# Optimization experiments

Hardware: AMD Instinct MI355X
Metric: run time of the kernel (lower is better)

The kernel has to match this reference:

```python
import jax, jax.numpy as jnp
import numpy as np

D, H, K, L, F, G, M, OUT = 1280, 16, 80, 4, 5120, 48, 2, 2048
HALF = K // 2  # rotary half dim = 40


def _token_coords(grid_thw, merge_size, N):
    tpi = grid_thw[:, 0] * grid_thw[:, 1] * grid_thw[:, 2]
    cu = jnp.concatenate([jnp.zeros(1, jnp.int32), jnp.cumsum(tpi).astype(jnp.int32)])
    tok = jnp.arange(N, dtype=jnp.int32)
    img_id = jnp.searchsorted(cu[1:], tok, side='right')
    local = tok - cu[img_id]
    h = grid_thw[img_id, 1]
    w = grid_thw[img_id, 2]
    spatial = local % (h * w)
    msq = merge_size * merge_size
    mw = w // merge_size
    group, intra = spatial // msq, spatial % msq
    row = (group // mw) * merge_size + intra // merge_size
    col = (group % mw) * merge_size + intra % merge_size
    return row, col, h, w, cu


def _layernorm(x, s, b, eps=1e-6):
    mu = jnp.mean(x, -1, keepdims=True)
    var = jnp.mean(jnp.square(x - mu), -1, keepdims=True)
    return (x - mu) * jax.lax.rsqrt(var + eps) * s + b


def _rotate_half(x):
    x1, x2 = x[..., :HALF], x[..., HALF:]
    return jnp.concatenate([-x2, x1], axis=-1)


def setup_inputs() -> dict:
    key = jax.random.key(0)
    ks = jax.random.split(key, 16)
    s = 0.02
    inp = {
        'pixels': jax.random.normal(ks[0], (2048, 1536), jnp.float32),
        'grid_thw': jnp.array([[1, 16, 32]] * 4, jnp.int32),
        'pos_embed': jax.random.normal(ks[1], (G * G, D), jnp.float32) * s,
        'patch_w': jax.random.normal(ks[2], (1536, D), jnp.float32) * s,
        'patch_b': jnp.zeros((D,), jnp.float32),
        'ln1_s': jnp.ones((L, D), jnp.float32), 'ln1_b': jnp.zeros((L, D), jnp.float32),
        'qkv_w': jax.random.normal(ks[3], (L, D, 3 * D), jnp.float32) * s,
        'qkv_b': jnp.zeros((L, 3 * D), jnp.float32),
        'proj_w': jax.random.normal(ks[4], (L, D, D), jnp.float32) * s,
        'proj_b': jnp.zeros((L, D), jnp.float32),
        'ln2_s': jnp.ones((L, D), jnp.float32), 'ln2_b': jnp.zeros((L, D), jnp.float32),
        'fc1_w': jax.random.normal(ks[5], (L, D, F), jnp.float32) * s,
        'fc1_b': jnp.zeros((L, F), jnp.float32),
        'fc2_w': jax.random.normal(ks[6], (L, F, D), jnp.float32) * s,
        'fc2_b': jnp.zeros((L, D), jnp.float32),
        'm_norm_s': jnp.ones((D,), jnp.float32), 'm_norm_b': jnp.zeros((D,), jnp.float32),
        'm_fc1_w': jax.random.normal(ks[7], (D * M * M, D * M * M), jnp.float32) * s,
        'm_fc1_b': jnp.zeros((D * M * M,), jnp.float32),
        'm_fc2_w': jax.random.normal(ks[8], (D * M * M, OUT), jnp.float32) * s,
        'm_fc2_b': jnp.zeros((OUT,), jnp.float32),
    }
    return inp


def _forward(pixels, grid_thw, pos_embed, patch_w, patch_b, ln1_s, ln1_b, qkv_w, qkv_b,
             proj_w, proj_b, ln2_s, ln2_b, fc1_w, fc1_b, fc2_w, fc2_b,
             m_norm_s, m_norm_b, m_fc1_w, m_fc1_b, m_fc2_w, m_fc2_b):
    N = pixels.shape[0]
    row, col, h, w, cu = _token_coords(grid_thw, M, N)

    # patch embed: conv with stride==kernel over flattened patches == linear
    x = pixels @ patch_w + patch_b  # [N, D]

    # bilinear position-embedding interpolation onto each image's (h, w) grid
    rf = jnp.where(h > 1, row.astype(jnp.float32) * (G - 1) / jnp.maximum(h - 1, 1), 0.0)
    cf = jnp.where(w > 1, col.astype(jnp.float32) * (G - 1) / jnp.maximum(w - 1, 1), 0.0)
    r0 = jnp.floor(rf).astype(jnp.int32); r1 = jnp.minimum(r0 + 1, G - 1)
    c0 = jnp.floor(cf).astype(jnp.int32); c1 = jnp.minimum(c0 + 1, G - 1)
    wr = (rf - r0)[:, None]; wc = (cf - c0)[:, None]
    pe = (pos_embed[r0 * G + c0] * (1 - wr) * (1 - wc)
          + pos_embed[r0 * G + c1] * (1 - wr) * wc
          + pos_embed[r1 * G + c0] * wr * (1 - wc)
          + pos_embed[r1 * G + c1] * wr * wc)
    x = x + pe

    # 2-D rotary embeddings
    inv_freq = 1.0 / (10000.0 ** (jnp.arange(0, HALF, 2, dtype=jnp.float32) / HALF))
    freqs = jnp.concatenate([row[:, None].astype(jnp.float32) * inv_freq,
                             col[:, None].astype(jnp.float32) * inv_freq], axis=-1)  # [N, HALF]
    emb = jnp.concatenate([freqs, freqs], axis=-1)  # [N, K]
    cos, sin = jnp.cos(emb)[:, None, :], jnp.sin(emb)[:, None, :]  # [N,1,K]

    # block-diagonal segment mask via cu_seqlens (N is a multiple of 128; no pad)
    tok = jnp.arange(N)
    seg = jnp.searchsorted(cu[1:], tok, side='right')
    k_start = cu[jnp.minimum(seg, cu.shape[0] - 2)]
    k_end = cu[jnp.minimum(seg + 1, cu.shape[0] - 1)]
    mask = (tok[None, :] >= k_start[:, None]) & (tok[None, :] < k_end[:, None])  # [N,N]
    scale = K ** -0.5

    for l in range(L):
        hdn = _layernorm(x, ln1_s[l], ln1_b[l])
        qkv = (hdn @ qkv_w[l] + qkv_b[l]).reshape(N, 3, H, K)
        q, k, v = qkv[:, 0], qkv[:, 1], qkv[:, 2]
        q = q * cos + _rotate_half(q) * sin
        k = k * cos + _rotate_half(k) * sin
        scores = jnp.einsum('nhk,mhk->hnm', q, k) * scale
        scores = jnp.where(mask[None], scores, jnp.finfo(scores.dtype).min)
        attn = jax.nn.softmax(scores, axis=-1)
        o = jnp.einsum('hnm,mhk->nhk', attn, v).reshape(N, D)
        x = x + o @ proj_w[l] + proj_b[l]

        hdn = _layernorm(x, ln2_s[l], ln2_b[l])
        ff = jax.nn.gelu(hdn @ fc1_w[l] + fc1_b[l], approximate=True)
        x = x + ff @ fc2_w[l] + fc2_b[l]

    # patch merger
    normed = _layernorm(x, m_norm_s, m_norm_b).reshape(N // (M * M), D * M * M)
    ff = jax.nn.gelu(normed @ m_fc1_w + m_fc1_b, approximate=True)
    return ff @ m_fc2_w + m_fc2_b  # [N/4, OUT]


def reference(pixels, grid_thw, pos_embed, patch_w, patch_b, ln1_s, ln1_b, qkv_w, qkv_b,
              proj_w, proj_b, ln2_s, ln2_b, fc1_w, fc1_b, fc2_w, fc2_b,
              m_norm_s, m_norm_b, m_fc1_w, m_fc1_b, m_fc2_w, m_fc2_b):
    return _forward(pixels, grid_thw, pos_embed, patch_w, patch_b, ln1_s, ln1_b, qkv_w, qkv_b,
                    proj_w, proj_b, ln2_s, ln2_b, fc1_w, fc1_b, fc2_w, fc2_b,
                    m_norm_s, m_norm_b, m_fc1_w, m_fc1_b, m_fc2_w, m_fc2_b)
```

## Files before the change

### kernel.cpp

```cpp
#include <hip/hip_runtime.h>
#include <math.h>

#define DMODEL 1280
#define NHEADS 16
#define FDIM   5120
#define GPOS   48
#define SEG    512

typedef __attribute__((ext_vector_type(8))) short bf16x8;
typedef __attribute__((ext_vector_type(4))) float f32x4;
typedef unsigned short u16;

__device__ __forceinline__ u16 f2bf(float f) {
  unsigned int u = __float_as_uint(f);
  u = (u + 0x7FFFu + ((u >> 16) & 1u)) >> 16;
  return (u16)u;
}
__device__ __forceinline__ float bf2f(u16 u) {
  return __uint_as_float((unsigned int)u << 16);
}
__device__ __forceinline__ float gelu_tanh(float x) {
  float u = 0.7978845608028654f * (x + 0.044715f * x * x * x);
  float t = __expf(2.f * u);
  float th = 1.f - 2.f / (t + 1.f);
  return 0.5f * x * (1.f + th);
}

typedef const __attribute__((address_space(1))) unsigned int* gas_t;
typedef __attribute__((address_space(3))) unsigned int* las_t;
__device__ __forceinline__ void async16(const void* g, void* l) {
  __builtin_amdgcn_global_load_lds((gas_t)g, (las_t)l, 16, 0, 0);
}

template <int EPI>
__global__ __launch_bounds__(256) void gemm_bt(
    const u16* __restrict__ A, const u16* __restrict__ B,
    const float* __restrict__ bias, void* __restrict__ Cv,
    int Kd, int lda, int ldb, int ldc, float scale,
    long long sA, long long sB, long long sC, int nsplit, long long pstride) {
  __shared__ __align__(16) u16 As[2][128 * 32];
  __shared__ __align__(16) u16 Bs[2][128 * 32];
  const int bz = blockIdx.z;
  const int bat = bz / nsplit, sp = bz - bat * nsplit;
  const int Ks = Kd / nsplit;
  const u16* Ab = A + (long long)bat * sA + (long long)sp * Ks;
  const u16* Bb = B + (long long)bat * sB + (long long)sp * Ks;
  const int m0 = blockIdx.x * 128, n0 = blockIdx.y * 128;
  const int t = threadIdx.x, ln = t & 63, w = t >> 6;
  const int srow = ln >> 2, scol = (ln & 3) * 8;
  const int m16 = ln & 15, q = ln >> 4;
  const int wr = w >> 1, wc = w & 1;

  f32x4 acc[4][4];
#pragma unroll
  for (int i = 0; i < 4; i++)
#pragma unroll
    for (int j = 0; j < 4; j++)
#pragma unroll
      for (int r = 0; r < 4; r++) acc[i][j][r] = 0.f;

  auto stage = [&](int k0, int p) {
#pragma unroll
    for (int it = 0; it < 2; it++) {
      int ra = it * 64 + w * 16;
      async16(Ab + (long long)(m0 + ra + srow) * lda + k0 + scol, &As[p][ra * 32]);
      async16(Bb + (long long)(n0 + ra + srow) * ldb + k0 + scol, &Bs[p][ra * 32]);
    }
  };

  stage(0, 0);
  int p = 0;
  for (int k0 = 0; k0 < Ks; k0 += 32) {
    __syncthreads();
    if (k0 + 32 < Ks) stage(k0 + 32, p ^ 1);
    bf16x8 av[4], bv[4];
#pragma unroll
    for (int mi = 0; mi < 4; mi++)
      av[mi] = *(const bf16x8*)&As[p][(wr * 64 + mi * 16 + m16) * 32 + q * 8];
#pragma unroll
    for (int ni = 0; ni < 4; ni++)
      bv[ni] = *(const bf16x8*)&Bs[p][(wc * 64 + ni * 16 + m16) * 32 + q * 8];
#pragma unroll
    for (int mi = 0; mi < 4; mi++)
#pragma unroll
      for (int ni = 0; ni < 4; ni++)
        acc[mi][ni] = __builtin_amdgcn_mfma_f32_16x16x32_bf16(
            av[mi], bv[ni], acc[mi][ni], 0, 0, 0);
    p ^= 1;
  }

#pragma unroll
  for (int mi = 0; mi < 4; mi++) {
#pragma unroll
    for (int r = 0; r < 4; r++) {
      int row = m0 + wr * 64 + mi * 16 + q * 4 + r;
      if (EPI == 0) {
        u16* Cp = (u16*)Cv + (long long)bat * sC +
                  (long long)sp * pstride + (long long)row * ldc;
#pragma unroll
        for (int ni = 0; ni < 4; ni++)
          Cp[n0 + wc * 64 + ni * 16 + m16] = f2bf(acc[mi][ni][r]);
      } else if (EPI == 2) {
        float* Cf = (float*)Cv + (long long)bat * sC + (long long)row * ldc;
#pragma unroll
        for (int ni = 0; ni < 4; ni++) {
          int col = n0 + wc * 64 + ni * 16 + m16;
          float v = acc[mi][ni][r] * scale;
          if (bias) v += bias[col];
          Cf[col] = v;
        }
      } else {
        u16* Cb = (u16*)Cv + (long long)bat * sC + (long long)row * ldc;
#pragma unroll
        for (int ni = 0; ni < 4; ni++) {
          int col = n0 + wc * 64 + ni * 16 + m16;
          float v = acc[mi][ni][r] + bias[col];
          if (EPI == 3) v = gelu_tanh(v);
          Cb[col] = f2bf(v);
        }
      }
    }
  }
}

#define STG256(mat, PW, ldx, h, kk, pp)                          \
  do {                                                           \
    const u16* g_ = (PW) + (long long)(h) * 128 * (ldx) + (kk);  \
    async16(g_, &L[pp][mat][h][(w * 2 + 0) * 512]);              \
    async16(g_ + 32, &L[pp][mat][h][(w * 2 + 1) * 512]);         \
  } while (0)

#define MM256(ii, ff)                                                          \
  acc[ii][ff] = __builtin_amdgcn_mfma_f32_16x16x32_bf16(aR[(ii) & 3][0],       \
                    bR[ff][0], acc[ii][ff], 0, 0, 0);                          \
  acc[ii][ff] = __builtin_amdgcn_mfma_f32_16x16x32_bf16(aR[(ii) & 3][1],       \
                    bR[ff][1], acc[ii][ff], 0, 0, 0);

#define BAR256() asm volatile("s_barrier" ::: "memory")
#define LGKM0() asm volatile("s_waitcnt lgkmcnt(0)" ::: "memory")

template <int EPI>
__global__ __launch_bounds__(512, 2) void gemm256(
    const u16* __restrict__ A, const u16* __restrict__ B,
    const float* __restrict__ bias, void* __restrict__ Cv,
    int Kd, int lda, int ldb, int ldc, int nsplit, long long pstride) {
  __shared__ __align__(16) u16 L[2][2][2][8192];
  const int sp = blockIdx.z;
  const int Ks = Kd / nsplit;
  const int NT = Ks >> 6;
  const u16* Ab = A + (long long)sp * Ks;
  const u16* Bb = B + (long long)sp * Ks;
  const int m0 = blockIdx.x * 256, n0 = blockIdx.y * 256;
  const int t = threadIdx.x, ln = t & 63, w = t >> 6;
  const int wr = w >> 2, wc = w & 3;
  const int m16 = ln & 15, q = ln >> 4;
  const int r16 = ln >> 2;
  const int csw = (ln & 3) ^ ((ln >> 5) << 1);
  const int rbase = m16 * 32 + (q ^ ((m16 >> 3) << 1)) * 8;

  const u16* Aw = Ab + (long long)(m0 + w * 16 + r16) * lda + csw * 8;
  const u16* Bw = Bb + (long long)(n0 + w * 16 + r16) * ldb + csw * 8;

  f32x4 acc[8][4];
#pragma unroll
  for (int i = 0; i < 8; i++)
#pragma unroll
    for (int j = 0; j < 4; j++)
#pragma unroll
      for (int r = 0; r < 4; r++) acc[i][j][r] = 0.f;

  STG256(0, Aw, lda, 0, 0, 0);
  STG256(0, Aw, lda, 1, 0, 0);
  STG256(1, Bw, ldb, 0, 0, 0);
  STG256(1, Bw, ldb, 1, 0, 0);
  if (NT > 1) {
    STG256(1, Bw, ldb, 0, 64, 1);
    STG256(1, Bw, ldb, 1, 64, 1);
    asm volatile("s_waitcnt vmcnt(4)" ::: "memory");
  } else {
    asm volatile("s_waitcnt vmcnt(0)" ::: "memory");
  }
  BAR256();

  const int wb = (wc & 1) * 4;
  for (int tt = 0; tt < NT; ++tt) {
    const int p = tt & 1;
    const u16* Abuf = &L[p][0][wr][0];
    const u16* Bbuf = &L[p][1][wc >> 1][0];
    bf16x8 aR[4][2], bR[4][2];

#pragma unroll
    for (int i = 0; i < 4; ++i) {
      aR[i][0] = *(const bf16x8*)(Abuf + (i * 2 + 0) * 512 + rbase);
      aR[i][1] = *(const bf16x8*)(Abuf + (i * 2 + 1) * 512 + rbase);
    }
#pragma unroll
    for (int fc = 0; fc < 2; ++fc) {
      bR[fc][0] = *(const bf16x8*)(Bbuf + ((wb + fc) * 2 + 0) * 512 + rbase);
      bR[fc][1] = *(const bf16x8*)(Bbuf + ((wb + fc) * 2 + 1) * 512 + rbase);
    }
    if (tt + 1 < NT) STG256(0, Aw, lda, 0, (tt + 1) * 64, (tt + 1) & 1);
    BAR256();
    LGKM0();
    __builtin_amdgcn_s_setprio(1);
#pragma unroll
    for (int i = 0; i < 4; ++i) { MM256(i, 0); MM256(i, 1); }
    __builtin_amdgcn_s_setprio(0);
    BAR256();

#pragma unroll
    for (int fc = 2; fc < 4; ++fc) {
      bR[fc][0] = *(const bf16x8*)(Bbuf + ((wb + fc) * 2 + 0) * 512 + rbase);
      bR[fc][1] = *(const bf16x8*)(Bbuf + ((wb + fc) * 2 + 1) * 512 + rbase);
    }
    if (tt + 1 < NT) STG256(0, Aw, lda, 1, (tt + 1) * 64, (tt + 1) & 1);
    BAR256();
    LGKM0();
    __builtin_amdgcn_s_setprio(1);
#pragma unroll
    for (int i = 0; i < 4; ++i) { MM256(i, 2); MM256(i, 3); }
    __builtin_amdgcn_s_setprio(0);
    BAR256();

#pragma unroll
    for (int i = 0; i < 4; ++i) {
      aR[i][0] = *(const bf16x8*)(Abuf + ((4 + i) * 2 + 0) * 512 + rbase);
      aR[i][1] = *(const bf16x8*)(Abuf + ((4 + i) * 2 + 1) * 512 + rbase);
    }
    if (tt + 2 < NT) STG256(1, Bw, ldb, 0, (tt + 2) * 64, p);
    BAR256();
    LGKM0();
    __builtin_amdgcn_s_setprio(1);
#pragma unroll
    for (int i = 0; i < 4; ++i) { MM256(4 + i, 2); MM256(4 + i, 3); }
    __builtin_amdgcn_s_setprio(0);
    BAR256();

    if (tt + 2 < NT) STG256(1, Bw, ldb, 1, (tt + 2) * 64, p);
    BAR256();
    LGKM0();
    __builtin_amdgcn_s_setprio(1);
#pragma unroll
    for (int i = 0; i < 4; ++i) { MM256(4 + i, 0); MM256(4 + i, 1); }
    __builtin_amdgcn_s_setprio(0);
    if (tt + 1 < NT) {
      if (tt + 2 < NT) asm volatile("s_waitcnt vmcnt(4)" ::: "memory");
      else             asm volatile("s_waitcnt vmcnt(0)" ::: "memory");
    }
    BAR256();
  }

#pragma unroll
  for (int fr = 0; fr < 8; fr++) {
#pragma unroll
    for (int r = 0; r < 4; r++) {
      int row = m0 + wr * 128 + fr * 16 + q * 4 + r;
      if (EPI == 0) {
        u16* Cp = (u16*)Cv + (long long)sp * pstride + (long long)row * ldc;
#pragma unroll
        for (int fc = 0; fc < 4; fc++)
          Cp[n0 + wc * 64 + fc * 16 + m16] = f2bf(acc[fr][fc][r]);
      } else {
        u16* Cb = (u16*)Cv + (long long)row * ldc;
#pragma unroll
        for (int fc = 0; fc < 4; fc++) {
          int col = n0 + wc * 64 + fc * 16 + m16;
          Cb[col] = f2bf(gelu_tanh(acc[fr][fc][r] + bias[col]));
        }
      }
    }
  }
}

template <int S, int RES, int GELU, int OUTBF>
__global__ void reduce_k(const u16* __restrict__ Pp, long long mn, int Nn,
                         const float* __restrict__ bias,
                         const float* __restrict__ res, void* __restrict__ out) {
  long long i = ((long long)blockIdx.x * 256 + threadIdx.x) * 4;
  if (i >= mn) return;
  float vx = 0.f, vy = 0.f, vz = 0.f, vw = 0.f;
#pragma unroll
  for (int s = 0; s < S; s++) {
    ushort4 u4 = *(const ushort4*)(Pp + (long long)s * mn + i);
    vx += bf2f(u4.x); vy += bf2f(u4.y); vz += bf2f(u4.z); vw += bf2f(u4.w);
  }
  int col = (int)(i % Nn);
  vx += bias[col]; vy += bias[col + 1]; vz += bias[col + 2]; vw += bias[col + 3];
  if (GELU) {
    vx = gelu_tanh(vx); vy = gelu_tanh(vy);
    vz = gelu_tanh(vz); vw = gelu_tanh(vw);
  }
  if (RES) {
    float4 r4 = *(const float4*)(res + i);
    vx += r4.x; vy += r4.y; vz += r4.z; vw += r4.w;
  }
  if (OUTBF) {
    ushort4 o; o.x = f2bf(vx); o.y = f2bf(vy); o.z = f2bf(vz); o.w = f2bf(vw);
    *(ushort4*)((u16*)out + i) = o;
  } else {
    float4 o; o.x = vx; o.y = vy; o.z = vz; o.w = vw;
    *(float4*)((float*)out + i) = o;
  }
}

__global__ void wconv_k(const float* __restrict__ in, u16* __restrict__ out,
                        int K, int N) {
  __shared__ float tl[32][33];
  int n0 = blockIdx.x * 32, k0 = blockIdx.y * 32;
  int t = threadIdx.x;
  int r = t >> 5, c = t & 31;
#pragma unroll
  for (int i = 0; i < 4; i++)
    tl[r + 8 * i][c] = in[(long long)(k0 + r + 8 * i) * N + n0 + c];
  __syncthreads();
  int n = t >> 4, kp = (t & 15) * 2;
#pragma unroll
  for (int i = 0; i < 2; i++) {
    ushort2 o;
    o.x = f2bf(tl[kp][n + 16 * i]);
    o.y = f2bf(tl[kp + 1][n + 16 * i]);
    *(ushort2*)&out[(long long)(n0 + n + 16 * i) * K + k0 + kp] = o;
  }
}

__global__ void conv_k(const float* __restrict__ in, u16* __restrict__ out,
                       long long n) {
  long long i = ((long long)blockIdx.x * 256 + threadIdx.x) * 4;
  if (i >= n) return;
  float4 v = *(const float4*)(in + i);
  ushort4 o; o.x = f2bf(v.x); o.y = f2bf(v.y); o.z = f2bf(v.z); o.w = f2bf(v.w);
  *(ushort4*)&out[i] = o;
}

union U16x8 { uint4 v; u16 s[8]; };
__global__ void vtr_k(const u16* __restrict__ in, u16* __restrict__ out) {
  __shared__ u16 tl[64][65];
  int b = blockIdx.z;
  int m0 = blockIdx.x * 64;
  int d0 = blockIdx.y * 64;
  const u16* ib = in + (long long)b * SEG * 128;
  u16* ob = out + (long long)b * 128 * SEG;
  int t = threadIdx.x;
  int r = t >> 3, c8 = (t & 7) * 8;
#pragma unroll
  for (int i = 0; i < 2; i++) {
    U16x8 ld;
    ld.v = *(const uint4*)&ib[(long long)(m0 + r + 32 * i) * 128 + d0 + c8];
#pragma unroll
    for (int j = 0; j < 8; j++) tl[r + 32 * i][c8 + j] = ld.s[j];
  }
  __syncthreads();
  int d = t >> 3, m8 = (t & 7) * 8;
#pragma unroll
  for (int i = 0; i < 2; i++) {
    int dd = d + 32 * i;
    U16x8 st;
#pragma unroll
    for (int j = 0; j < 8; j++) st.s[j] = tl[m8 + j][dd];
    *(uint4*)&ob[(long long)(d0 + dd) * SEG + m0 + m8] = st.v;
  }
}

__global__ void coords_k(const int* __restrict__ g, int nimg,
                         int* __restrict__ rw, int* __restrict__ cl,
                         int* __restrict__ hh, int* __restrict__ ww, int N) {
  int t = blockIdx.x * 256 + threadIdx.x;
  if (t >= N) return;
  int c = 0, local = 0, H = 1, W = 1;
  for (int i = 0; i < nimg; i++) {
    int tpi = g[i * 3] * g[i * 3 + 1] * g[i * 3 + 2];
    if (t >= c && t < c + tpi) { local = t - c; H = g[i * 3 + 1]; W = g[i * 3 + 2]; }
    c += tpi;
  }
  int hw = H * W;
  int sp = local % hw;
  int mw = W >> 1;
  int gr = sp >> 2, intra = sp & 3;
  rw[t] = (gr / mw) * 2 + (intra >> 1);
  cl[t] = (gr % mw) * 2 + (intra & 1);
  hh[t] = H; ww[t] = W;
}

__global__ void peadd_k(float* __restrict__ x, const float* __restrict__ pe,
                        const int* __restrict__ rw, const int* __restrict__ cl,
                        const int* __restrict__ hh, const int* __restrict__ ww) {
  int n = blockIdx.x;
  int d = threadIdx.x * 4;
  int H = hh[n], W = ww[n];
  float rf = (H > 1) ? (float)rw[n] * (float)(GPOS - 1) / (float)(H - 1) : 0.f;
  float cf = (W > 1) ? (float)cl[n] * (float)(GPOS - 1) / (float)(W - 1) : 0.f;
  int r0 = (int)floorf(rf), c0 = (int)floorf(cf);
  int r1 = min(r0 + 1, GPOS - 1), c1 = min(c0 + 1, GPOS - 1);
  float wr = rf - (float)r0, wc = cf - (float)c0;
  float w00 = (1.f - wr) * (1.f - wc), w01 = (1.f - wr) * wc;
  float w10 = wr * (1.f - wc), w11 = wr * wc;
  float4 v00 = *(const float4*)(pe + (long long)(r0 * GPOS + c0) * DMODEL + d);
  float4 v01 = *(const float4*)(pe + (long long)(r0 * GPOS + c1) * DMODEL + d);
  float4 v10 = *(const float4*)(pe + (long long)(r1 * GPOS + c0) * DMODEL + d);
  float4 v11 = *(const float4*)(pe + (long long)(r1 * GPOS + c1) * DMODEL + d);
  float4 xv = *(float4*)(x + (long long)n * DMODEL + d);
  xv.x += w00 * v00.x + w01 * v01.x + w10 * v10.x + w11 * v11.x;
  xv.y += w00 * v00.y + w01 * v01.y + w10 * v10.y + w11 * v11.y;
  xv.z += w00 * v00.z + w01 * v01.z + w10 * v10.z + w11 * v11.z;
  xv.w += w00 * v00.w + w01 * v01.w + w10 * v10.w + w11 * v11.w;
  *(float4*)(x + (long long)n * DMODEL + d) = xv;
}

__global__ void ln_k(const float* __restrict__ X, u16* __restrict__ Y,
                     const float* __restrict__ s, const float* __restrict__ b) {
  int row = blockIdx.x;
  int d = threadIdx.x * 4;
  const float* x = X + (long long)row * DMODEL;
  float4 v = *(const float4*)(x + d);
  float sum = v.x + v.y + v.z + v.w;
#pragma unroll
  for (int o = 32; o; o >>= 1) sum += __shfl_xor(sum, o);
  __shared__ float red[8];
  int wv = threadIdx.x >> 6, lnn = threadIdx.x & 63;
  if (lnn == 0) red[wv] = sum;
  __syncthreads();
  float mu = 0.f;
  for (int i = 0; i < 5; i++) mu += red[i];
  mu *= (1.f / DMODEL);
  float dx = v.x - mu, dy = v.y - mu, dz = v.z - mu, dw = v.w - mu;
  float s2 = dx * dx + dy * dy + dz * dz + dw * dw;
#pragma unroll
  for (int o = 32; o; o >>= 1) s2 += __shfl_xor(s2, o);
  __syncthreads();
  if (lnn == 0) red[wv] = s2;
  __syncthreads();
  float var = 0.f;
  for (int i = 0; i < 5; i++) var += red[i];
  var *= (1.f / DMODEL);
  float rs = rsqrtf(var + 1e-6f);
  ushort4 o4;
  o4.x = f2bf(dx * rs * s[d] + b[d]);
  o4.y = f2bf(dy * rs * s[d + 1] + b[d + 1]);
  o4.z = f2bf(dz * rs * s[d + 2] + b[d + 2]);
  o4.w = f2bf(dw * rs * s[d + 3] + b[d + 3]);
  *(ushort4*)(Y + (long long)row * DMODEL + d) = o4;
}

__global__ void rope_k(const u16* __restrict__ qkv, const int* __restrict__ rw,
                       const int* __restrict__ cl, u16* __restrict__ qr,
                       u16* __restrict__ kr, u16* __restrict__ vp, int N) {
  int n = blockIdx.x, h = blockIdx.y, t = threadIdx.x;
  const u16* src = qkv + (long long)n * (3 * DMODEL) + h * 80;
  long long ob96 = ((long long)h * N + n) * 96;
  long long ob128 = ((long long)h * N + n) * 128;
  if (t < 40) {
    float pos = (t < 20) ? (float)rw[n] : (float)cl[n];
    float infr = exp2f(-13.287712379549449f * (float)(t % 20) * 0.05f);
    float f = pos * infr;
    float cs = cosf(f), sn = sinf(f);
    float q0 = bf2f(src[t]), q1 = bf2f(src[t + 40]);
    qr[ob96 + t] = f2bf(q0 * cs - q1 * sn);
    qr[ob96 + t + 40] = f2bf(q1 * cs + q0 * sn);
    float k0 = bf2f(src[DMODEL + t]), k1 = bf2f(src[DMODEL + t + 40]);
    kr[ob96 + t] = f2bf(k0 * cs - k1 * sn);
    kr[ob96 + t + 40] = f2bf(k1 * cs + k0 * sn);
    vp[ob128 + t] = src[2 * DMODEL + t];
    vp[ob128 + t + 40] = src[2 * DMODEL + t + 40];
  } else {
    int u = t - 40;
    if (u < 16) { qr[ob96 + 80 + u] = 0; kr[ob96 + 80 + u] = 0; }
    vp[ob128 + 80 + u] = 0;
    vp[ob128 + 104 + u] = 0;
  }
}

__global__ void softmax_k(const float* __restrict__ sc, u16* __restrict__ P) {
  long long base = ((long long)blockIdx.y * SEG + blockIdx.x) * SEG;
  int t = threadIdx.x;
  float4 a = *(const float4*)(sc + base + t * 4);
  float4 b = *(const float4*)(sc + base + 256 + t * 4);
  float mx = fmaxf(fmaxf(fmaxf(a.x, a.y), fmaxf(a.z, a.w)),
                   fmaxf(fmaxf(b.x, b.y), fmaxf(b.z, b.w)));
#pragma unroll
  for (int o = 32; o; o >>= 1) mx = fmaxf(mx, __shfl_xor(mx, o));
  a.x = __expf(a.x - mx); a.y = __expf(a.y - mx);
  a.z = __expf(a.z - mx); a.w = __expf(a.w - mx);
  b.x = __expf(b.x - mx); b.y = __expf(b.y - mx);
  b.z = __expf(b.z - mx); b.w = __expf(b.w - mx);
  float sm = a.x + a.y + a.z + a.w + b.x + b.y + b.z + b.w;
#pragma unroll
  for (int o = 32; o; o >>= 1) sm += __shfl_xor(sm, o);
  float r = 1.f / sm;
  ushort4 oa, ob;
  oa.x = f2bf(a.x * r); oa.y = f2bf(a.y * r); oa.z = f2bf(a.z * r); oa.w = f2bf(a.w * r);
  ob.x = f2bf(b.x * r); ob.y = f2bf(b.y * r); ob.z = f2bf(b.z * r); ob.w = f2bf(b.w * r);
  *(ushort4*)(P + base + t * 4) = oa;
  *(ushort4*)(P + base + 256 + t * 4) = ob;
}

__global__ void repack_k(const u16* __restrict__ op, u16* __restrict__ o, int N) {
  int id = blockIdx.x * 256 + threadIdx.x;
  if (id >= N * DMODEL) return;
  int n = id / DMODEL, c = id % DMODEL;
  int h = c / 80, kk = c % 80;
  int seg = n >> 9, m = n & (SEG - 1);
  long long base = (long long)(h * 4 + seg) * (2 * SEG * 128) + (long long)m * 128 + kk;
  o[id] = f2bf(bf2f(op[base]) + bf2f(op[base + SEG * 128]));
}

static void gemm(hipStream_t st, int epi, const u16* A, const u16* B,
                 const float* bias, void* C, int M, int Nn, int Kd, int lda,
                 int ldb, int ldc, float scale, long long sA, long long sB,
                 long long sC, int batches, int nsplit) {
  dim3 g(M / 128, Nn / 128, batches * nsplit), blk(256);
  long long ps = (long long)M * Nn;
  switch (epi) {
    case 0: gemm_bt<0><<<g, blk, 0, st>>>(A, B, bias, C, Kd, lda, ldb, ldc, scale, sA, sB, sC, nsplit, ps); break;
    case 1: gemm_bt<1><<<g, blk, 0, st>>>(A, B, bias, C, Kd, lda, ldb, ldc, scale, sA, sB, sC, nsplit, ps); break;
    case 2: gemm_bt<2><<<g, blk, 0, st>>>(A, B, bias, C, Kd, lda, ldb, ldc, scale, sA, sB, sC, nsplit, ps); break;
    default: gemm_bt<3><<<g, blk, 0, st>>>(A, B, bias, C, Kd, lda, ldb, ldc, scale, sA, sB, sC, nsplit, ps); break;
  }
}

static void gemm_big(hipStream_t st, int epi, const u16* A, const u16* B,
                     const float* bias, void* C, int M, int Nn, int Kd,
                     int lda, int ldb, int ldc, int nsplit) {
  dim3 g(M / 256, Nn / 256, nsplit), blk(512);
  long long ps = (long long)M * Nn;
  if (epi == 0)
    gemm256<0><<<g, blk, 0, st>>>(A, B, nullptr, C, Kd, lda, ldb, ldc, nsplit, ps);
  else
    gemm256<3><<<g, blk, 0, st>>>(A, B, bias, C, Kd, lda, ldb, ldc, nsplit, ps);
}

extern "C" void kernel_launch(void* const* d_in, const int* in_sizes, int n_in,
                              void* d_out, int out_size, void* d_ws, size_t ws_size,
                              hipStream_t stream) {
  const float* pixels = (const float*)d_in[0];
  const int* grid_thw = (const int*)d_in[1];
  const float* pos_embed = (const float*)d_in[2];
  const float* patch_w = (const float*)d_in[3];
  const float* patch_b = (const float*)d_in[4];
  const float* ln1_s = (const float*)d_in[5];
  const float* ln1_b = (const float*)d_in[6];
  const float* qkv_w = (const float*)d_in[7];
  const float* qkv_b = (const float*)d_in[8];
  const float* proj_w = (const float*)d_in[9];
  const float* proj_b = (const float*)d_in[10];
  const float* ln2_s = (const float*)d_in[11];
  const float* ln2_b = (const float*)d_in[12];
  const float* fc1_w = (const float*)d_in[13];
  const float* fc1_b = (const float*)d_in[14];
  const float* fc2_w = (const float*)d_in[15];
  const float* fc2_b = (const float*)d_in[16];
  const float* mns = (const float*)d_in[17];
  const float* mnb = (const float*)d_in[18];
  const float* mf1w = (const float*)d_in[19];
  const float* mf1b = (const float*)d_in[20];
  const float* mf2w = (const float*)d_in[21];
  const float* mf2b = (const float*)d_in[22];
  float* out = (float*)d_out;

  const int N = in_sizes[0] / 1536;
  const int nimg = in_sizes[1] / 3;
  const int nseg = N / SEG;
  const int nb = NHEADS * nseg;

  char* w = (char*)d_ws;
  size_t off = 0;
  auto alloc = [&](size_t bytes) -> void* {
    void* p = w + off;
    off += (bytes + 255) & ~(size_t)255;
    return p;
  };
  int* rw = (int*)alloc((size_t)N * 4);
  int* cl = (int*)alloc((size_t)N * 4);
  int* hh = (int*)alloc((size_t)N * 4);
  int* ww = (int*)alloc((size_t)N * 4);
  float* x = (float*)alloc((size_t)N * DMODEL * 4);
  u16* h = (u16*)alloc((size_t)N * DMODEL * 2);
  u16* pixbf = (u16*)alloc((size_t)N * 1536 * 2);
  u16* patchT = (u16*)alloc((size_t)DMODEL * 1536 * 2);
  u16* qkvT = (u16*)alloc((size_t)3 * DMODEL * DMODEL * 2);
  u16* projT = (u16*)alloc((size_t)DMODEL * DMODEL * 2);
  u16* fc1T = (u16*)alloc((size_t)FDIM * DMODEL * 2);
  u16* fc2T = (u16*)alloc((size_t)DMODEL * FDIM * 2);
  u16* qkvb = (u16*)alloc((size_t)N * 3 * DMODEL * 2);
  u16* qr = (u16*)alloc((size_t)NHEADS * N * 96 * 2);
  u16* kr = (u16*)alloc((size_t)NHEADS * N * 96 * 2);
  u16* vp = (u16*)alloc((size_t)NHEADS * N * 128 * 2);
  u16* vpT = (u16*)alloc((size_t)NHEADS * N * 128 * 2);
  u16* op = (u16*)alloc((size_t)nb * 2 * SEG * 128 * 2);
  u16* o = (u16*)alloc((size_t)N * DMODEL * 2);
  float* bigA = (float*)alloc((size_t)nb * SEG * SEG * 4);
  float* bigB = (float*)alloc((size_t)nb * SEG * SEG * 2);
  (void)ws_size;
  u16* mfc1T = qkvb;
  u16* mfc2T = pixbf;
  u16* ffb = (u16*)bigA;
  u16* mf = (u16*)bigA;
  u16* P = (u16*)bigB;
  u16* part = (u16*)bigB;

  const float iscale = 0.11180339887498949f;

  coords_k<<<dim3((N + 255) / 256), 256, 0, stream>>>(grid_thw, nimg, rw, cl, hh, ww, N);
  conv_k<<<dim3((int)(((long long)N * 1536 / 4 + 255) / 256)), 256, 0, stream>>>(
      pixels, pixbf, (long long)N * 1536);
  wconv_k<<<dim3(DMODEL / 32, 1536 / 32), 256, 0, stream>>>(patch_w, patchT, 1536, DMODEL);
  gemm_big(stream, 0, pixbf, patchT, nullptr, part, N, DMODEL, 1536, 1536, 1536,
           DMODEL, 4);
  reduce_k<4, 0, 0, 0><<<dim3((int)(((long long)N * DMODEL / 4 + 255) / 256)), 256, 0, stream>>>(
      part, (long long)N * DMODEL, DMODEL, patch_b, nullptr, x);
  peadd_k<<<dim3(N), 320, 0, stream>>>(x, pos_embed, rw, cl, hh, ww);

  for (int l = 0; l < 4; l++) {
    wconv_k<<<dim3(3 * DMODEL / 32, DMODEL / 32), 256, 0, stream>>>(
        qkv_w + (size_t)l * DMODEL * 3 * DMODEL, qkvT, DMODEL, 3 * DMODEL);
    wconv_k<<<dim3(DMODEL / 32, DMODEL / 32), 256, 0, stream>>>(
        proj_w + (size_t)l * DMODEL * DMODEL, projT, DMODEL, DMODEL);
    wconv_k<<<dim3(FDIM / 32, DMODEL / 32), 256, 0, stream>>>(
        fc1_w + (size_t)l * DMODEL * FDIM, fc1T, DMODEL, FDIM);
    wconv_k<<<dim3(DMODEL / 32, FDIM / 32), 256, 0, stream>>>(
        fc2_w + (size_t)l * FDIM * DMODEL, fc2T, FDIM, DMODEL);

    ln_k<<<dim3(N), 320, 0, stream>>>(x, h, ln1_s + l * DMODEL, ln1_b + l * DMODEL);
    gemm_big(stream, 0, h, qkvT, nullptr, part, N, 3 * DMODEL, DMODEL,
             DMODEL, DMODEL, 3 * DMODEL, 2);
    reduce_k<2, 0, 0, 1><<<dim3((int)(((long long)N * 3 * DMODEL / 4 + 255) / 256)), 256, 0, stream>>>(
        part, (long long)N * 3 * DMODEL, 3 * DMODEL, qkv_b + (size_t)l * 3 * DMODEL,
        nullptr, qkvb);
    rope_k<<<dim3(N, NHEADS), 64, 0, stream>>>(qkvb, rw, cl, qr, kr, vp, N);
    gemm(stream, 2, qr, kr, nullptr, bigA, SEG, SEG, 96, 96, 96, SEG, iscale,
         (long long)SEG * 96, (long long)SEG * 96, (long long)SEG * SEG, nb, 1);
    softmax_k<<<dim3(SEG, nb), 64, 0, stream>>>(bigA, P);
    vtr_k<<<dim3(8, 2, nb), 256, 0, stream>>>(vp, vpT);
    gemm(stream, 0, P, vpT, nullptr, op, SEG, 128, SEG, SEG, SEG, 128, 1.f,
         (long long)SEG * SEG, (long long)128 * SEG, (long long)2 * SEG * 128, nb, 2);
    repack_k<<<dim3((N * DMODEL + 255) / 256), 256, 0, stream>>>(op, o, N);
    gemm_big(stream, 0, o, projT, nullptr, part, N, DMODEL, DMODEL, DMODEL,
             DMODEL, DMODEL, 4);
    reduce_k<4, 1, 0, 0><<<dim3((int)(((long long)N * DMODEL / 4 + 255) / 256)), 256, 0, stream>>>(
        part, (long long)N * DMODEL, DMODEL, proj_b + (size_t)l * DMODEL, x, x);
    ln_k<<<dim3(N), 320, 0, stream>>>(x, h, ln2_s + l * DMODEL, ln2_b + l * DMODEL);
    gemm_big(stream, 3, h, fc1T, fc1_b + (size_t)l * FDIM, ffb, N, FDIM, DMODEL,
             DMODEL, DMODEL, FDIM, 1);
    gemm_big(stream, 0, ffb, fc2T, nullptr, part, N, DMODEL, FDIM, FDIM, FDIM,
             DMODEL, 4);
    reduce_k<4, 1, 0, 0><<<dim3((int)(((long long)N * DMODEL / 4 + 255) / 256)), 256, 0, stream>>>(
        part, (long long)N * DMODEL, DMODEL, fc2_b + (size_t)l * DMODEL, x, x);
  }

  ln_k<<<dim3(N), 320, 0, stream>>>(x, h, mns, mnb);
  const int Mm = N / 4;
  wconv_k<<<dim3(FDIM / 32, FDIM / 32), 256, 0, stream>>>(mf1w, mfc1T, FDIM, FDIM);
  gemm_big(stream, 0, h, mfc1T, nullptr, part, Mm, FDIM, FDIM, FDIM, FDIM, FDIM, 4);
  reduce_k<4, 0, 1, 1><<<dim3((int)(((long long)Mm * FDIM / 4 + 255) / 256)), 256, 0, stream>>>(
      part, (long long)Mm * FDIM, FDIM, mf1b, nullptr, mf);
  wconv_k<<<dim3(2048 / 32, FDIM / 32), 256, 0, stream>>>(mf2w, mfc2T, FDIM, 2048);
  gemm_big(stream, 0, mf, mfc2T, nullptr, part, Mm, 2048, FDIM, FDIM, FDIM, 2048, 16);
  reduce_k<16, 0, 0, 0><<<dim3((int)(((long long)Mm * 2048 / 4 + 255) / 256)), 256, 0, stream>>>(
      part, (long long)Mm * 2048, 2048, mf2b, nullptr, out);
}
```

Baseline: 1.587 ms.

## Fuse attention into flash-style kernel and add bias epilogue to QKV GEMM

Replaces the per-segment score GEMM, separate softmax, PV GEMM with split-K and repack with a single fused attention kernel. It uses online softmax in registers, double-buffered async K/V staging in shared memory, and writes the head output directly in token-major layout. Separately, the QKV GEMM now runs without split-K and adds bias in a new epilogue, dropping its reduce pass. This removes several launches and the fp32 score matrix round trip through global memory. In exchange, the attention grid is small (4 x 64 blocks) and the QKV GEMM has less parallelism.

```diff
diff --git a/kernel.cpp b/kernel.cpp
--- a/kernel.cpp
+++ b/kernel.cpp
@@ -260,6 +260,13 @@
 #pragma unroll
         for (int fc = 0; fc < 4; fc++)
           Cp[n0 + wc * 64 + fc * 16 + m16] = f2bf(acc[fr][fc][r]);
+      } else if (EPI == 1) {
+        u16* Cb = (u16*)Cv + (long long)row * ldc;
+#pragma unroll
+        for (int fc = 0; fc < 4; fc++) {
+          int col = n0 + wc * 64 + fc * 16 + m16;
+          Cb[col] = f2bf(acc[fr][fc][r] + bias[col]);
+        }
       } else {
         u16* Cb = (u16*)Cv + (long long)row * ldc;
 #pragma unroll
@@ -268,6 +275,156 @@
           Cb[col] = f2bf(gelu_tanh(acc[fr][fc][r] + bias[col]));
         }
       }
+    }
+  }
+}
+
+__global__ __launch_bounds__(256) void fattn_k(
+    const u16* __restrict__ qr, const u16* __restrict__ kr,
+    const u16* __restrict__ vpT, u16* __restrict__ o, int N, float iscale) {
+  __shared__ __align__(16) u16 Ks[2][24][512];
+  __shared__ __align__(16) u16 Vs[2][20][512];
+  __shared__ __align__(16) u16 Ps[4][32 * 128];
+  const int nseg = N >> 9;
+  const int hb = blockIdx.y;
+  const int h = hb / nseg, seg = hb - h * nseg;
+  const int t = threadIdx.x, ln = t & 63, w = t >> 6;
+  const int m16 = ln & 15, qh = ln >> 4;
+  const int r4 = ln >> 2, gsw = (ln & 3) ^ ((ln >> 5) << 1);
+  const int rbase = m16 * 32 + ((qh ^ ((m16 >> 3) << 1)) << 3);
+  const long long hN = (long long)h * N;
+  const int segbase = seg * SEG;
+  const int q0 = segbase + blockIdx.x * 128 + w * 32;
+
+  bf16x8 qf[2][3];
+#pragma unroll
+  for (int mi = 0; mi < 2; mi++)
+#pragma unroll
+    for (int ks = 0; ks < 3; ks++)
+      qf[mi][ks] = *(const bf16x8*)&qr[(hN + q0 + mi * 16 + m16) * 96 + ks * 32 + qh * 8];
+
+  f32x4 ao[2][5];
+#pragma unroll
+  for (int mi = 0; mi < 2; mi++)
+#pragma unroll
+    for (int df = 0; df < 5; df++)
+#pragma unroll
+      for (int r = 0; r < 4; r++) ao[mi][df][r] = 0.f;
+  float m_[2][4], l_[2][4];
+#pragma unroll
+  for (int mi = 0; mi < 2; mi++)
+#pragma unroll
+    for (int r = 0; r < 4; r++) { m_[mi][r] = -1e30f; l_[mi][r] = 0.f; }
+
+  auto stage = [&](int c, int pb) {
+#pragma unroll
+    for (int i = 0; i < 6; i++) {
+      int sK = w * 6 + i, f = sK / 3, kg = sK - f * 3;
+      async16(&kr[(hN + segbase + c * 128 + f * 16 + r4) * 96 + kg * 32 + gsw * 8],
+              &Ks[pb][sK][0]);
+    }
+#pragma unroll
+    for (int i = 0; i < 5; i++) {
+      int sV = w * 5 + i, df = sV >> 2, kvg = sV & 3;
+      async16(&vpT[((long long)hb * 128 + df * 16 + r4) * SEG + c * 128 + kvg * 32 + gsw * 8],
+              &Vs[pb][sV][0]);
+    }
+  };
+
+  stage(0, 0);
+  u16* Pmy = &Ps[w][0];
+  for (int c = 0; c < 4; c++) {
+    const int pb = c & 1;
+    __syncthreads();
+    if (c < 3) stage(c + 1, pb ^ 1);
+
+    f32x4 s[2][8];
+#pragma unroll
+    for (int mi = 0; mi < 2; mi++)
+#pragma unroll
+      for (int f = 0; f < 8; f++)
+#pragma unroll
+        for (int r = 0; r < 4; r++) s[mi][f][r] = 0.f;
+#pragma unroll
+    for (int ks = 0; ks < 3; ks++) {
+#pragma unroll
+      for (int f = 0; f < 8; f++) {
+        bf16x8 kf = *(const bf16x8*)&Ks[pb][f * 3 + ks][rbase];
+#pragma unroll
+        for (int mi = 0; mi < 2; mi++)
+          s[mi][f] = __builtin_amdgcn_mfma_f32_16x16x32_bf16(qf[mi][ks], kf, s[mi][f], 0, 0, 0);
+      }
+    }
+
+#pragma unroll
+    for (int mi = 0; mi < 2; mi++) {
+#pragma unroll
+      for (int r = 0; r < 4; r++) {
+        float mx = s[mi][0][r];
+#pragma unroll
+        for (int f = 1; f < 8; f++) mx = fmaxf(mx, s[mi][f][r]);
+        mx *= iscale;
+#pragma unroll
+        for (int o2 = 1; o2 <= 8; o2 <<= 1) mx = fmaxf(mx, __shfl_xor(mx, o2));
+        float mn = fmaxf(m_[mi][r], mx);
+        float corr = __expf(m_[mi][r] - mn);
+        m_[mi][r] = mn;
+        float rs = 0.f;
+#pragma unroll
+        for (int f = 0; f < 8; f++) {
+          float p = __expf(s[mi][f][r] * iscale - mn);
+          s[mi][f][r] = p;
+          rs += p;
+        }
+#pragma unroll
+        for (int o2 = 1; o2 <= 8; o2 <<= 1) rs += __shfl_xor(rs, o2);
+        l_[mi][r] = l_[mi][r] * corr + rs;
+#pragma unroll
+        for (int df = 0; df < 5; df++) ao[mi][df][r] *= corr;
+      }
+    }
+
+#pragma unroll
+    for (int mi = 0; mi < 2; mi++) {
+#pragma unroll
+      for (int r = 0; r < 4; r++) {
+        int qq = mi * 16 + qh * 4 + r;
+        int base = qq * 128 + (m16 & 7);
+        int ql = qq & 7;
+#pragma unroll
+        for (int f = 0; f < 8; f++) {
+          int gr = (f * 2 + (m16 >> 3)) ^ ql;
+          Pmy[base + gr * 8] = f2bf(s[mi][f][r]);
+        }
+      }
+    }
+
+#pragma unroll
+    for (int ks = 0; ks < 4; ks++) {
+      bf16x8 pf[2];
+#pragma unroll
+      for (int mi = 0; mi < 2; mi++)
+        pf[mi] = *(const bf16x8*)&Pmy[(mi * 16 + m16) * 128 +
+                                      (((ks * 4 + qh) ^ (m16 & 7)) << 3)];
+#pragma unroll
+      for (int df = 0; df < 5; df++) {
+        bf16x8 vf = *(const bf16x8*)&Vs[pb][df * 4 + ks][rbase];
+#pragma unroll
+        for (int mi = 0; mi < 2; mi++)
+          ao[mi][df] = __builtin_amdgcn_mfma_f32_16x16x32_bf16(pf[mi], vf, ao[mi][df], 0, 0, 0);
+      }
+    }
+  }
+
+#pragma unroll
+  for (int mi = 0; mi < 2; mi++) {
+#pragma unroll
+    for (int r = 0; r < 4; r++) {
+      float rl = 1.f / l_[mi][r];
+      long long rowb = (long long)(q0 + mi * 16 + qh * 4 + r) * DMODEL + h * 80;
+#pragma unroll
+      for (int df = 0; df < 5; df++)
+        o[rowb + df * 16 + m16] = f2bf(ao[mi][df][r] * rl);
     }
   }
 }
@@ -469,40 +626,6 @@
   }
 }
 
-__global__ void softmax_k(const float* __restrict__ sc, u16* __restrict__ P) {
-  long long base = ((long long)blockIdx.y * SEG + blockIdx.x) * SEG;
-  int t = threadIdx.x;
-  float4 a = *(const float4*)(sc + base + t * 4);
-  float4 b = *(const float4*)(sc + base + 256 + t * 4);
-  float mx = fmaxf(fmaxf(fmaxf(a.x, a.y), fmaxf(a.z, a.w)),
-                   fmaxf(fmaxf(b.x, b.y), fmaxf(b.z, b.w)));
-#pragma unroll
-  for (int o = 32; o; o >>= 1) mx = fmaxf(mx, __shfl_xor(mx, o));
-  a.x = __expf(a.x - mx); a.y = __expf(a.y - mx);
-  a.z = __expf(a.z - mx); a.w = __expf(a.w - mx);
-  b.x = __expf(b.x - mx); b.y = __expf(b.y - mx);
-  b.z = __expf(b.z - mx); b.w = __expf(b.w - mx);
-  float sm = a.x + a.y + a.z + a.w + b.x + b.y + b.z + b.w;
-#pragma unroll
-  for (int o = 32; o; o >>= 1) sm += __shfl_xor(sm, o);
-  float r = 1.f / sm;
-  ushort4 oa, ob;
-  oa.x = f2bf(a.x * r); oa.y = f2bf(a.y * r); oa.z = f2bf(a.z * r); oa.w = f2bf(a.w * r);
-  ob.x = f2bf(b.x * r); ob.y = f2bf(b.y * r); ob.z = f2bf(b.z * r); ob.w = f2bf(b.w * r);
-  *(ushort4*)(P + base + t * 4) = oa;
-  *(ushort4*)(P + base + 256 + t * 4) = ob;
-}
-
-__global__ void repack_k(const u16* __restrict__ op, u16* __restrict__ o, int N) {
-  int id = blockIdx.x * 256 + threadIdx.x;
-  if (id >= N * DMODEL) return;
-  int n = id / DMODEL, c = id % DMODEL;
-  int h = c / 80, kk = c % 80;
-  int seg = n >> 9, m = n & (SEG - 1);
-  long long base = (long long)(h * 4 + seg) * (2 * SEG * 128) + (long long)m * 128 + kk;
-  o[id] = f2bf(bf2f(op[base]) + bf2f(op[base + SEG * 128]));
-}
-
 static void gemm(hipStream_t st, int epi, const u16* A, const u16* B,
                  const float* bias, void* C, int M, int Nn, int Kd, int lda,
                  int ldb, int ldc, float scale, long long sA, long long sB,
@@ -522,10 +645,11 @@
                      int lda, int ldb, int ldc, int nsplit) {
   dim3 g(M / 256, Nn / 256, nsplit), blk(512);
   long long ps = (long long)M * Nn;
-  if (epi == 0)
-    gemm256<0><<<g, blk, 0, st>>>(A, B, nullptr, C, Kd, lda, ldb, ldc, nsplit, ps);
-  else
-    gemm256<3><<<g, blk, 0, st>>>(A, B, bias, C, Kd, lda, ldb, ldc, nsplit, ps);
+  switch (epi) {
+    case 0: gemm256<0><<<g, blk, 0, st>>>(A, B, bias, C, Kd, lda, ldb, ldc, nsplit, ps); break;
+    case 1: gemm256<1><<<g, blk, 0, st>>>(A, B, bias, C, Kd, lda, ldb, ldc, nsplit, ps); break;
+    default: gemm256<3><<<g, blk, 0, st>>>(A, B, bias, C, Kd, lda, ldb, ldc, nsplit, ps); break;
+  }
 }
 
 extern "C" void kernel_launch(void* const* d_in, const int* in_sizes, int n_in,
@@ -585,16 +709,15 @@
   u16* kr = (u16*)alloc((size_t)NHEADS * N * 96 * 2);
   u16* vp = (u16*)alloc((size_t)NHEADS * N * 128 * 2);
   u16* vpT = (u16*)alloc((size_t)NHEADS * N * 128 * 2);
-  u16* op = (u16*)alloc((size_t)nb * 2 * SEG * 128 * 2);
+  u16* pad0 = (u16*)alloc((size_t)nb * 2 * SEG * 128 * 2);
   u16* o = (u16*)alloc((size_t)N * DMODEL * 2);
   float* bigA = (float*)alloc((size_t)nb * SEG * SEG * 4);
   float* bigB = (float*)alloc((size_t)nb * SEG * SEG * 2);
-  (void)ws_size;
+  (void)ws_size; (void)pad0;
   u16* mfc1T = qkvb;
   u16* mfc2T = pixbf;
   u16* ffb = (u16*)bigA;
   u16* mf = (u16*)bigA;
-  u16* P = (u16*)bigB;
   u16* part = (u16*)bigB;
 
   const float iscale = 0.11180339887498949f;
@@ -620,19 +743,11 @@
         fc2_w + (size_t)l * FDIM * DMODEL, fc2T, FDIM, DMODEL);
 
     ln_k<<<dim3(N), 320, 0, stream>>>(x, h, ln1_s + l * DMODEL, ln1_b + l * DMODEL);
-    gemm_big(stream, 0, h, qkvT, nullptr, part, N, 3 * DMODEL, DMODEL,
-             DMODEL, DMODEL, 3 * DMODEL, 2);
-    reduce_k<2, 0, 0, 1><<<dim3((int)(((long long)N * 3 * DMODEL / 4 + 255) / 256)), 256, 0, stream>>>(
-        part, (long long)N * 3 * DMODEL, 3 * DMODEL, qkv_b + (size_t)l * 3 * DMODEL,
-        nullptr, qkvb);
+    gemm_big(stream, 1, h, qkvT, qkv_b + (size_t)l * 3 * DMODEL, qkvb, N,
+             3 * DMODEL, DMODEL, DMODEL, DMODEL, 3 * DMODEL, 1);
     rope_k<<<dim3(N, NHEADS), 64, 0, stream>>>(qkvb, rw, cl, qr, kr, vp, N);
-    gemm(stream, 2, qr, kr, nullptr, bigA, SEG, SEG, 96, 96, 96, SEG, iscale,
-         (long long)SEG * 96, (long long)SEG * 96, (long long)SEG * SEG, nb, 1);
-    softmax_k<<<dim3(SEG, nb), 64, 0, stream>>>(bigA, P);
     vtr_k<<<dim3(8, 2, nb), 256, 0, stream>>>(vp, vpT);
-    gemm(stream, 0, P, vpT, nullptr, op, SEG, 128, SEG, SEG, SEG, 128, 1.f,
-         (long long)SEG * SEG, (long long)128 * SEG, (long long)2 * SEG * 128, nb, 2);
-    repack_k<<<dim3((N * DMODEL + 255) / 256), 256, 0, stream>>>(op, o, N);
+    fattn_k<<<dim3(SEG / 128, nb), 256, 0, stream>>>(qr, kr, vpT, o, N, iscale);
     gemm_big(stream, 0, o, projT, nullptr, part, N, DMODEL, DMODEL, DMODEL,
              DMODEL, DMODEL, 4);
     reduce_k<4, 1, 0, 0><<<dim3((int)(((long long)N * DMODEL / 4 + 255) / 256)), 256, 0, stream>>>(
```

Measured after the change: 1.485 ms. -6.4%, faster.
